# Kernel tuning notes

Measured on AMD Instinct MI355X. Metric: run time of the kernel, lower is better.

## Reference

```python
import jax, jax.numpy as jnp
import numpy as np

B, S, D = 4, 4096, 1024

def setup_inputs() -> dict:
    key = jax.random.key(0)
    ks = jax.random.split(key, 8)
    scale = 1.0 / np.sqrt(D)
    return {
        "inputs": jax.random.normal(ks[0], (B, S, D), dtype=jnp.float32),
        "context": jax.random.normal(ks[1], (B, S, D), dtype=jnp.float32),
        "Wq": jax.random.normal(ks[2], (D, D), dtype=jnp.float32) * scale,
        "bq": jnp.zeros((D,), dtype=jnp.float32),
        "Wk": jax.random.normal(ks[3], (D, D), dtype=jnp.float32) * scale,
        "bk": jnp.zeros((D,), dtype=jnp.float32),
        "Wv": jax.random.normal(ks[4], (D, D), dtype=jnp.float32) * scale,
        "bv": jnp.zeros((D,), dtype=jnp.float32),
        "Wo": jax.random.normal(ks[5], (D, D), dtype=jnp.float32) * scale,
        "bo": jnp.zeros((D,), dtype=jnp.float32),
    }

def reference(inputs, context, Wq, bq, Wk, bk, Wv, bv, Wo, bo):
    phi = lambda x: jax.nn.elu(x) + 1.0
    q_phi = phi(jnp.einsum("bsd,de->bse", inputs, Wq) + bq)   # [B,S,D]
    k_phi = phi(jnp.einsum("bsd,de->bse", context, Wk) + bk)  # [B,S,D]
    v = jnp.einsum("bsd,de->bse", context, Wv) + bv           # [B,S,D]
    kv = jnp.einsum("bsd,bse->bde", k_phi, v)                 # [B,D,D]
    k_sum = jnp.sum(k_phi, axis=1)                            # [B,D]
    z = 1.0 / (jnp.einsum("bsd,bd->bs", q_phi, k_sum)[..., None] + 1e-6)  # [B,S,1]
    out = jnp.einsum("bsd,bde->bse", q_phi, kv) * z           # [B,S,D]
    return jnp.einsum("bsd,de->bse", out, Wo) + bo + inputs
```

## Files before the change

### kernel.cpp

```cpp
#include <hip/hip_runtime.h>


typedef __bf16 bf16x8 __attribute__((ext_vector_type(8)));
typedef __bf16 bf16x4 __attribute__((ext_vector_type(4)));
typedef float  f32x4  __attribute__((ext_vector_type(4)));

#define GLOBAL_AS __attribute__((address_space(1)))
#define LDS_AS    __attribute__((address_space(3)))

#define SS 4096
#define DD 1024

__device__ __forceinline__ __bf16 f2bf(float f) {
  union { float f; unsigned u; } a; a.f = f;
  unsigned r = a.u + 0x7FFFu + ((a.u >> 16) & 1u);
  union { unsigned short s; __bf16 b; } o; o.s = (unsigned short)(r >> 16);
  return o.b;
}

__device__ __forceinline__ void async_load16(const void* g, void* l) {
  __builtin_amdgcn_global_load_lds((const GLOBAL_AS void*)g, (LDS_AS void*)l, 16, 0, 0);
}


#define LA0 0
#define LA1 16384
#define LB0 32768
#define LB1 49152

#define VMW(n)  asm volatile("s_waitcnt vmcnt(" #n ")" ::: "memory")
#define SBAR()  asm volatile("s_barrier" ::: "memory")
#define LGK0()  do { asm volatile("s_waitcnt lgkmcnt(0)" ::: "memory"); \
                     __builtin_amdgcn_sched_barrier(0); } while (0)

#define STG_A(BASE, mh, kt) do {                                              \
    async_load16(Aa + (long)((mh)*64 + t6) * K + (kt)*64 + gc8,               \
                 smem + (BASE) + (mh)*8192 + tid*8);                          \
    async_load16(Aa + (long)(128 + (mh)*64 + t6) * K + (kt)*64 + gc8,         \
                 smem + (BASE) + (mh)*8192 + 4096 + tid*8);                   \
  } while (0)

#define STG_B(BASE, nh, kt) do {                                              \
    async_load16(Bb + (long)(tA*64 + (nh)*32 + t5) * K + (kt)*64 + gc8,       \
                 smem + (BASE) + (nh)*8192 + tid*8);                          \
    async_load16(Bb + (long)(128 + tA*64 + (nh)*32 + t5) * K + (kt)*64 + gc8, \
                 smem + (BASE) + (nh)*8192 + 4096 + tid*8);                   \
  } while (0)

#define RD_A(dst, AB, mh)                                                     \
    _Pragma("unroll") for (int rr = 0; rr < 4; ++rr) {                        \
      const int o = (AB) + (mh)*8192 + rr*1024 + aoff;                        \
      dst[rr][0] = *(const bf16x8*)(smem + o);                                \
      dst[rr][1] = *(const bf16x8*)(smem + (o ^ 32));                         \
    }

#define RD_B(dst, BB, nh)                                                     \
    _Pragma("unroll") for (int nn = 0; nn < 2; ++nn) {                        \
      const int o = (BB) + (nh)*8192 + nn*1024 + boff;                        \
      dst[nn][0] = *(const bf16x8*)(smem + o);                                \
      dst[nn][1] = *(const bf16x8*)(smem + (o ^ 32));                         \
    }

#define MM(mh, nh, af, bf)                                                    \
    __builtin_amdgcn_s_setprio(1);                                            \
    _Pragma("unroll") for (int rr = 0; rr < 4; ++rr)                          \
    _Pragma("unroll") for (int nn = 0; nn < 2; ++nn) {                        \
      acc[(mh)*4+rr][(nh)*2+nn] = __builtin_amdgcn_mfma_f32_16x16x32_bf16(    \
          af[rr][0], bf[nn][0], acc[(mh)*4+rr][(nh)*2+nn], 0, 0, 0);          \
      acc[(mh)*4+rr][(nh)*2+nn] = __builtin_amdgcn_mfma_f32_16x16x32_bf16(    \
          af[rr][1], bf[nn][1], acc[(mh)*4+rr][(nh)*2+nn], 0, 0, 0);          \
    }                                                                         \
    __builtin_amdgcn_s_setprio(0)

#define PH(VM, RDS, STG, MMM) do {                                            \
    VM; RDS; STG;                                                             \
    SBAR();                                                                   \
    LGK0();                                                                   \
    MMM;                                                                      \
    SBAR();                                                                   \
  } while (0)

template<int MODE>
__global__ __launch_bounds__(512, 2)
void gemm256(const __bf16* __restrict__ Ag, const __bf16* __restrict__ Bg,
             void* __restrict__ Cg, void* __restrict__ Cg2,
             int N, int K, long sB,
             const float* __restrict__ bias, const float* __restrict__ bias2,
             const float* __restrict__ zvec, const float* __restrict__ resid)
{
  union SMem {
    __bf16 st[65536];
    __bf16 T[256 * 136];
  };
  __shared__ SMem sm;
  __bf16* smem = sm.st;

  int bx = blockIdx.x, by = blockIdx.y;
  {
    const int gx = gridDim.x, gy = gridDim.y;
    if ((gy & 7) == 0) {
      const int f = by * gx + bx;
      const int j = f & 7;
      const int u = f >> 3;
      bx = u % gx;
      by = j * (gy >> 3) + u / gx;
    }
  }

  const int tid  = threadIdx.x;
  const int lane = tid & 63, wave = tid >> 6;
  const int wm   = wave >> 2, wn = wave & 3;
  const int ln   = lane & 15, quad = lane >> 4;
  const int t6   = tid >> 3, tA = t6 >> 5, t5 = t6 & 31;
  const int gc8  = ((tid & 7) ^ (t6 & 7)) * 8;
  const int pco  = (quad ^ (ln & 7)) * 8;
  const int aoff = (wm * 64 + ln) * 64 + pco;
  const int boff = (wn * 32 + ln) * 64 + pco;

  const long m0  = (long)by * 256;
  const int  n0g = bx * 256;
  const __bf16* Aa = Ag + m0 * K;
  const __bf16* Bb = Bg + (long)bx * 256 * K +
                     ((MODE == 8) ? (long)(m0 >> 12) * sB : 0);

  f32x4 acc[8][4];
  const f32x4 zero = {0.f, 0.f, 0.f, 0.f};
#pragma unroll
  for (int i = 0; i < 8; i++)
#pragma unroll
    for (int j = 0; j < 4; j++) acc[i][j] = zero;

  STG_A(LA0, 0, 0); STG_B(LB0, 0, 0);
  STG_A(LA0, 1, 0); STG_B(LB0, 1, 0);
  STG_A(LA1, 0, 1); STG_B(LB1, 0, 1);
  VMW(8);
  SBAR();

  const int niter = K >> 7;
#pragma unroll 1
  for (int i = 0; i < niter - 1; ++i) {
    const int kb = i * 2;
    bf16x8 a[4][2], b[2][2], b1[2][2];
    PH(VMW(4), RD_A(a, LA0, 0) RD_B(b, LB0, 0), STG_A(LA1, 1, kb + 1), MM(0, 0, a, b));
    PH(      , RD_B(b1, LB0, 1),                STG_B(LB1, 1, kb + 1), MM(0, 1, a, b1));
    PH(      , RD_A(a, LA0, 1) RD_B(b, LB0, 0), STG_A(LA0, 0, kb + 2), MM(1, 0, a, b));
    PH(VMW(6), RD_B(b1, LB0, 1),                STG_B(LB0, 0, kb + 2), MM(1, 1, a, b1));
    PH(VMW(4), RD_A(a, LA1, 0) RD_B(b, LB1, 0), STG_A(LA0, 1, kb + 2), MM(0, 0, a, b));
    PH(      , RD_B(b1, LB1, 1),                STG_B(LB0, 1, kb + 2), MM(0, 1, a, b1));
    PH(      , RD_A(a, LA1, 1) RD_B(b, LB1, 0), STG_A(LA1, 0, kb + 3), MM(1, 0, a, b));
    PH(VMW(6), RD_B(b1, LB1, 1),                STG_B(LB1, 0, kb + 3), MM(1, 1, a, b1));
  }
  {
    const int kb = (niter - 1) * 2;
    bf16x8 a[4][2], b[2][2], b1[2][2];
    PH(VMW(4), RD_A(a, LA0, 0) RD_B(b, LB0, 0), STG_A(LA1, 1, kb + 1), MM(0, 0, a, b));
    PH(      , RD_B(b1, LB0, 1),                STG_B(LB1, 1, kb + 1), MM(0, 1, a, b1));
    PH(      , RD_A(a, LA0, 1) RD_B(b, LB0, 0), ,                      MM(1, 0, a, b));
    PH(VMW(0), RD_B(b1, LB0, 1),                ,                      MM(1, 1, a, b1));
    PH(      , RD_A(a, LA1, 0) RD_B(b, LB1, 0), ,                      MM(0, 0, a, b));
    PH(      , RD_B(b1, LB1, 1),                ,                      MM(0, 1, a, b1));
    PH(      , RD_A(a, LA1, 1) RD_B(b, LB1, 0), ,                      MM(1, 0, a, b));
    PH(      , RD_B(b1, LB1, 1),                ,                      MM(1, 1, a, b1));
  }

  if (MODE == 6) {
    const bool isK = (n0g < 1024);
    const float* bb = isK ? bias : bias2;
    const int nb = isK ? n0g : (n0g - 1024);
    const int b = (int)(m0 >> 12);
    const long s_in = m0 & 4095;
    __bf16* dst = (__bf16*)(isK ? Cg : Cg2) + (long)b * DD * SS;
#pragma unroll
    for (int h = 0; h < 2; ++h) {
      if (wm == h) {
#pragma unroll
        for (int mf = 0; mf < 8; ++mf)
#pragma unroll
          for (int nf = 0; nf < 4; ++nf) {
            const int nl = wn * 64 + nf * 16 + ln;
            const int sl0 = mf * 16 + quad * 4;
            const float bv = bb[nb + nl];
            bf16x4 pk;
#pragma unroll
            for (int r = 0; r < 4; ++r) {
              float x = acc[mf][nf][r] + bv;
              if (isK) x = (x > 0.f) ? (x + 1.f) : __expf(x);
              pk[r] = f2bf(x);
            }
            *(bf16x4*)(sm.T + nl * 136 + sl0) = pk;
          }
      }
      __syncthreads();
#pragma unroll
      for (int p2 = 0; p2 < 8; ++p2) {
        const int row = (tid >> 4) + p2 * 32;
        const int c   = (tid & 15) * 8;
        bf16x8 vv = *(const bf16x8*)(sm.T + row * 136 + c);
        *(bf16x8*)&dst[(long)(nb + row) * SS + s_in + h * 128 + c] = vv;
      }
      __syncthreads();
    }
    return;
  }

#pragma unroll
  for (int mf = 0; mf < 8; ++mf)
#pragma unroll
    for (int nf = 0; nf < 4; ++nf)
#pragma unroll
      for (int r = 0; r < 4; ++r) {
        const long gm = m0 + wm * 128 + mf * 16 + quad * 4 + r;
        const int  gn = n0g + wn * 64 + nf * 16 + ln;
        float x = acc[mf][nf][r];
        if (MODE == 0) {
          x += bias[gn];
          x = (x > 0.f) ? (x + 1.f) : __expf(x);
          ((__bf16*)Cg)[gm * (long)N + gn] = f2bf(x);
        } else {
          x = x * zvec[gm] + bias[gn];
          ((float*)Cg)[gm * (long)N + gn] = x + resid[gm * (long)N + gn];
        }
      }
}

#undef PH
#undef MM
#undef RD_A
#undef RD_B
#undef STG_A
#undef STG_B

template<int MODE>
__global__ __launch_bounds__(256)
void gemm_bt(const __bf16* __restrict__ Ag, const __bf16* __restrict__ Bg,
             void* __restrict__ Cg, void* __restrict__ Cg2,
             int N, int K, long sA, long sB, long sC,
             const float* __restrict__ bias, const float* __restrict__ bias2,
             const float* __restrict__ zvec,
             const float* __restrict__ resid)
{
  union SMem {
    struct { __bf16 As[128 * 64]; __bf16 Bs[128 * 64]; } s;
    __bf16 T[128 * 136];
  };
  __shared__ SMem sm;

  int bx = blockIdx.x, by = blockIdx.y;
  {
    const int gx = gridDim.x, gy = gridDim.y;
    if ((gy & 7) == 0) {
      const int f = by * gx + bx;
      const int j = f & 7;
      const int u = f >> 3;
      bx = u % gx;
      by = j * (gy >> 3) + u / gx;
    }
  }
  int bz = blockIdx.z;
  int k0beg = 0, k0end = K;
  if (MODE == 5) {
    const int split = bz & 3;
    bz >>= 2;
    k0beg = split * (K >> 2);
    k0end = k0beg + (K >> 2);
  }

  const int tid = threadIdx.x;
  const long m0 = (long)by * 128;
  const __bf16* A = Ag + m0 * K + bz * sA;
  const __bf16* B = Bg + (long)bx * 128 * K + bz * sB;

  const int srow = tid >> 3;
  const int gcc8 = ((tid & 7) ^ (srow & 7)) * 8;

  const int lane = tid & 63;
  const int wave = tid >> 6;
  const int wm   = (wave >> 1) * 64;
  const int wn   = (wave & 1) * 64;
  const int ln   = lane & 15;
  const int quad = lane >> 4;
  const int rk   = ln & 7;

  f32x4 acc[4][4];
  const f32x4 zero = {0.f, 0.f, 0.f, 0.f};
#pragma unroll
  for (int i = 0; i < 4; i++)
#pragma unroll
    for (int j = 0; j < 4; j++) acc[i][j] = zero;

  for (int k0 = k0beg; k0 < k0end; k0 += 64) {
#pragma unroll
    for (int p = 0; p < 4; p++) {
      async_load16(A + (long)(p * 32 + srow) * K + k0 + gcc8, sm.s.As + p * 2048 + tid * 8);
      async_load16(B + (long)(p * 32 + srow) * K + k0 + gcc8, sm.s.Bs + p * 2048 + tid * 8);
    }
    __syncthreads();

#pragma unroll
    for (int ksub = 0; ksub < 2; ksub++) {
      const int cc = (ksub * 4 + quad) ^ rk;
      bf16x8 af[4], bfr[4];
#pragma unroll
      for (int i = 0; i < 4; i++)
        af[i] = *(const bf16x8*)(sm.s.As + (wm + i * 16 + ln) * 64 + cc * 8);
#pragma unroll
      for (int j = 0; j < 4; j++)
        bfr[j] = *(const bf16x8*)(sm.s.Bs + (wn + j * 16 + ln) * 64 + cc * 8);
#pragma unroll
      for (int i = 0; i < 4; i++)
#pragma unroll
        for (int j = 0; j < 4; j++)
          acc[i][j] = __builtin_amdgcn_mfma_f32_16x16x32_bf16(af[i], bfr[j], acc[i][j], 0, 0, 0);
    }
    __syncthreads();
  }

  const int n0g = bx * 128;
#pragma unroll
  for (int i = 0; i < 4; i++) {
#pragma unroll
    for (int j = 0; j < 4; j++) {
#pragma unroll
      for (int r = 0; r < 4; r++) {
        const int lrow = wm + i * 16 + quad * 4 + r;
        const int lcol = wn + j * 16 + ln;
        const long gm  = m0 + lrow;
        const int  gn  = n0g + lcol;
        float x = acc[i][j][r];
        if (MODE == 5) {
          __hip_atomic_fetch_add(&((float*)Cg)[(long)bz * sC + gm * (long)N + gn],
                                 x, __ATOMIC_RELAXED, __HIP_MEMORY_SCOPE_AGENT);
        } else if (MODE == 7) {
          ((__bf16*)Cg)[(long)bz * sC + gm * (long)N + gn] = f2bf(x);
        }
      }
    }
  }
}

__global__ __launch_bounds__(256)
void cvt_f32_bf16(const float* __restrict__ x, __bf16* __restrict__ y, long n)
{
  long i = ((long)blockIdx.x * 256 + threadIdx.x) * 4;
  if (i < n) {
    float4 v = *(const float4*)(x + i);
    bf16x4 o;
    o[0] = f2bf(v.x); o[1] = f2bf(v.y); o[2] = f2bf(v.z); o[3] = f2bf(v.w);
    *(bf16x4*)(y + i) = o;
  }
}

__global__ __launch_bounds__(256)
void wtrans(const float* W0, const float* W1, const float* W2, const float* W3,
            __bf16* O0, __bf16* O1, __bf16* O2, __bf16* O3, int Dd)
{
  __shared__ __bf16 t[64][72];
  const float* W = (blockIdx.z == 0) ? W0 : (blockIdx.z == 1) ? W1 : (blockIdx.z == 2) ? W2 : W3;
  __bf16*      O = (blockIdx.z == 0) ? O0 : (blockIdx.z == 1) ? O1 : (blockIdx.z == 2) ? O2 : O3;
  const int r0 = blockIdx.y * 64, c0 = blockIdx.x * 64;
  const int tid = threadIdx.x;
  const int lr4 = tid >> 4, lc4 = (tid & 15) * 4;
#pragma unroll
  for (int it = 0; it < 4; it++) {
    const int row = lr4 + it * 16;
    float4 v = *(const float4*)&W[(long)(r0 + row) * Dd + c0 + lc4];
    t[row][lc4 + 0] = f2bf(v.x);
    t[row][lc4 + 1] = f2bf(v.y);
    t[row][lc4 + 2] = f2bf(v.z);
    t[row][lc4 + 3] = f2bf(v.w);
  }
  __syncthreads();
  const int lr8 = tid >> 3, lc8 = (tid & 7) * 8;
#pragma unroll
  for (int it = 0; it < 2; it++) {
    const int orow = lr8 + it * 32;
    bf16x8 vb;
#pragma unroll
    for (int j = 0; j < 8; j++) vb[j] = t[lc8 + j][orow];
    *(bf16x8*)&O[(long)(c0 + orow) * Dd + r0 + lc8] = vb;
  }
}

__global__ __launch_bounds__(256)
void ksum_k(const __bf16* __restrict__ kphiT, float* __restrict__ ksum, int S)
{
  const long row = blockIdx.x;
  const __bf16* p = kphiT + row * (long)S;
  const int tid = threadIdx.x;
  float s = 0.f;
  for (int j = tid * 8; j < S; j += 256 * 8) {
    bf16x8 v = *(const bf16x8*)&p[j];
#pragma unroll
    for (int e = 0; e < 8; e++) s += (float)v[e];
  }
  __shared__ float red[256];
  red[tid] = s; __syncthreads();
  for (int off = 128; off > 0; off >>= 1) {
    if (tid < off) red[tid] += red[tid + off];
    __syncthreads();
  }
  if (tid == 0) ksum[row] = red[0];
}

__global__ __launch_bounds__(256)
void zden_k(const __bf16* __restrict__ qphi, const float* __restrict__ ksum,
            float* __restrict__ z, int Dd, int S)
{
  const long row = blockIdx.x;
  const int  b   = (int)(row / S);
  const __bf16* q = qphi + row * (long)Dd;
  const float* ks = ksum + (long)b * Dd;
  const int tid = threadIdx.x;
  const int i = tid * 4;
  bf16x4 qv = *(const bf16x4*)&q[i];
  float4 kv4 = *(const float4*)&ks[i];
  float s = (float)qv[0] * kv4.x + (float)qv[1] * kv4.y +
            (float)qv[2] * kv4.z + (float)qv[3] * kv4.w;
  __shared__ float red[256];
  red[tid] = s; __syncthreads();
  for (int off = 128; off > 0; off >>= 1) {
    if (tid < off) red[tid] += red[tid + off];
    __syncthreads();
  }
  if (tid == 0) z[row] = 1.f / (red[0] + 1e-6f);
}

extern "C" void kernel_launch(void* const* d_in, const int* in_sizes, int n_in,
                              void* d_out, int out_size, void* d_ws, size_t ws_size,
                              hipStream_t stream)
{
  const float* inputs  = (const float*)d_in[0];
  const float* context = (const float*)d_in[1];
  const float* Wq = (const float*)d_in[2];
  const float* bq = (const float*)d_in[3];
  const float* Wk = (const float*)d_in[4];
  const float* bk = (const float*)d_in[5];
  const float* Wv = (const float*)d_in[6];
  const float* bv = (const float*)d_in[7];
  const float* Wo = (const float*)d_in[8];
  const float* bo = (const float*)d_in[9];
  float* out = (float*)d_out;

  const int Bn = 4;
  const long NSD = (long)Bn * SS * DD;
  const long MB = 1L << 20;

  char* ws = (char*)d_ws;
  __bf16* xbf   = (__bf16*)(ws + 0 * MB);
  __bf16* cbf   = (__bf16*)(ws + 32 * MB);
  __bf16* qphi  = (__bf16*)(ws + 64 * MB);
  __bf16* kphiT = (__bf16*)(ws + 96 * MB);
  __bf16* vT    = (__bf16*)(ws + 128 * MB);
  float*  kvf   = (float*)(ws + 160 * MB);
  __bf16* kvbf  = (__bf16*)(ws + 176 * MB);
  __bf16* M2T   = (__bf16*)(ws + 184 * MB);
  __bf16* WqT   = (__bf16*)(ws + 192 * MB);
  __bf16* WkT   = (__bf16*)(ws + 194 * MB);
  __bf16* WvT   = (__bf16*)(ws + 196 * MB);
  __bf16* WoT   = (__bf16*)(ws + 198 * MB);
  float*  ksum  = (float*)(ws + 200 * MB);
  float*  zbuf  = (float*)(ws + 201 * MB);

  cvt_f32_bf16<<<16384, 256, 0, stream>>>(inputs,  xbf, NSD);
  cvt_f32_bf16<<<16384, 256, 0, stream>>>(context, cbf, NSD);
  wtrans<<<dim3(16, 16, 4), 256, 0, stream>>>(Wq, Wk, Wv, Wo, WqT, WkT, WvT, WoT, DD);

  gemm256<0><<<dim3(4, 64), 512, 0, stream>>>(xbf, WqT, qphi, nullptr,
      DD, DD, 0, bq, nullptr, nullptr, nullptr);

  gemm256<6><<<dim3(8, 64), 512, 0, stream>>>(cbf, WkT, kphiT, vT,
      2048, DD, 0, bk, bv, nullptr, nullptr);

  ksum_k<<<4096, 256, 0, stream>>>(kphiT, ksum, SS);
  zden_k<<<16384, 256, 0, stream>>>(qphi, ksum, zbuf, DD, SS);

  hipMemsetAsync(kvf, 0, (size_t)Bn * DD * DD * sizeof(float), stream);
  gemm_bt<5><<<dim3(8, 8, 16), 256, 0, stream>>>(kphiT, vT, kvf, nullptr,
      DD, SS, (long)DD * SS, (long)DD * SS, (long)DD * DD,
      nullptr, nullptr, nullptr, nullptr);
  cvt_f32_bf16<<<4096, 256, 0, stream>>>(kvf, kvbf, (long)Bn * DD * DD);

  gemm_bt<7><<<dim3(8, 8, 4), 256, 0, stream>>>(WoT, kvbf, M2T, nullptr,
      DD, DD, 0, (long)DD * DD, (long)DD * DD, nullptr, nullptr, nullptr, nullptr);

  gemm256<8><<<dim3(4, 64), 512, 0, stream>>>(qphi, M2T, out, nullptr,
      DD, DD, (long)DD * DD, bo, nullptr, zbuf, inputs);
}
```

Measured before the change: 512.2 us.

## Halve GEMM main-loop barriers and reorder MFMA phases to reuse B fragments

The main loop and tail of the bf16 GEMM drop the trailing s_barrier and the explicit lgkmcnt(0)/sched_barrier from each phase, so each phase has one barrier. Async global-to-LDS staging is now issued before the LDS fragment reads. The MFMA sub-tile order in each half-iteration becomes (0,0),(0,1),(1,1),(1,0), so the B fragments already in registers are reused and two RD_B reloads per half-iteration are skipped. The goal is to cut barrier stalls and LDS read traffic. The risk is a write-after-read race on LDS buffers now that the second barrier is gone, plus less control over instruction scheduling.

```diff
diff --git a/kernel.cpp b/kernel.cpp
--- a/kernel.cpp
+++ b/kernel.cpp
@@ -30,8 +30,6 @@
 
 #define VMW(n)  asm volatile("s_waitcnt vmcnt(" #n ")" ::: "memory")
 #define SBAR()  asm volatile("s_barrier" ::: "memory")
-#define LGK0()  do { asm volatile("s_waitcnt lgkmcnt(0)" ::: "memory"); \
-                     __builtin_amdgcn_sched_barrier(0); } while (0)
 
 #define STG_A(BASE, mh, kt) do {                                              \
     async_load16(Aa + (long)((mh)*64 + t6) * K + (kt)*64 + gc8,               \
@@ -72,12 +70,10 @@
     }                                                                         \
     __builtin_amdgcn_s_setprio(0)
 
-#define PH(VM, RDS, STG, MMM) do {                                            \
-    VM; RDS; STG;                                                             \
+#define PH(VM, STG, RDS, MMM) do {                                            \
+    VM; STG; RDS;                                                             \
     SBAR();                                                                   \
-    LGK0();                                                                   \
     MMM;                                                                      \
-    SBAR();                                                                   \
   } while (0)
 
 template<int MODE>
@@ -141,26 +137,27 @@
   for (int i = 0; i < niter - 1; ++i) {
     const int kb = i * 2;
     bf16x8 a[4][2], b[2][2], b1[2][2];
-    PH(VMW(4), RD_A(a, LA0, 0) RD_B(b, LB0, 0), STG_A(LA1, 1, kb + 1), MM(0, 0, a, b));
-    PH(      , RD_B(b1, LB0, 1),                STG_B(LB1, 1, kb + 1), MM(0, 1, a, b1));
-    PH(      , RD_A(a, LA0, 1) RD_B(b, LB0, 0), STG_A(LA0, 0, kb + 2), MM(1, 0, a, b));
-    PH(VMW(6), RD_B(b1, LB0, 1),                STG_B(LB0, 0, kb + 2), MM(1, 1, a, b1));
-    PH(VMW(4), RD_A(a, LA1, 0) RD_B(b, LB1, 0), STG_A(LA0, 1, kb + 2), MM(0, 0, a, b));
-    PH(      , RD_B(b1, LB1, 1),                STG_B(LB0, 1, kb + 2), MM(0, 1, a, b1));
-    PH(      , RD_A(a, LA1, 1) RD_B(b, LB1, 0), STG_A(LA1, 0, kb + 3), MM(1, 0, a, b));
-    PH(VMW(6), RD_B(b1, LB1, 1),                STG_B(LB1, 0, kb + 3), MM(1, 1, a, b1));
+    PH(VMW(4), STG_A(LA1,1,kb+1), RD_A(a,LA0,0) RD_B(b,LB0,0), MM(0,0,a,b));
+    PH(      , STG_B(LB1,1,kb+1), RD_B(b1,LB0,1),              MM(0,1,a,b1));
+    PH(      , STG_A(LA0,0,kb+2), RD_A(a,LA0,1),               MM(1,1,a,b1));
+    PH(VMW(6), STG_B(LB0,0,kb+2), ,                            MM(1,0,a,b));
+    PH(VMW(4), STG_A(LA0,1,kb+2), RD_A(a,LA1,0) RD_B(b,LB1,0), MM(0,0,a,b));
+    PH(      , STG_B(LB0,1,kb+2), RD_B(b1,LB1,1),              MM(0,1,a,b1));
+    PH(      , STG_A(LA1,0,kb+3), RD_A(a,LA1,1),               MM(1,1,a,b1));
+    PH(VMW(6), STG_B(LB1,0,kb+3), ,                            MM(1,0,a,b));
   }
   {
     const int kb = (niter - 1) * 2;
     bf16x8 a[4][2], b[2][2], b1[2][2];
-    PH(VMW(4), RD_A(a, LA0, 0) RD_B(b, LB0, 0), STG_A(LA1, 1, kb + 1), MM(0, 0, a, b));
-    PH(      , RD_B(b1, LB0, 1),                STG_B(LB1, 1, kb + 1), MM(0, 1, a, b1));
-    PH(      , RD_A(a, LA0, 1) RD_B(b, LB0, 0), ,                      MM(1, 0, a, b));
-    PH(VMW(0), RD_B(b1, LB0, 1),                ,                      MM(1, 1, a, b1));
-    PH(      , RD_A(a, LA1, 0) RD_B(b, LB1, 0), ,                      MM(0, 0, a, b));
-    PH(      , RD_B(b1, LB1, 1),                ,                      MM(0, 1, a, b1));
-    PH(      , RD_A(a, LA1, 1) RD_B(b, LB1, 0), ,                      MM(1, 0, a, b));
-    PH(      , RD_B(b1, LB1, 1),                ,                      MM(1, 1, a, b1));
+    PH(VMW(4), STG_A(LA1,1,kb+1), RD_A(a,LA0,0) RD_B(b,LB0,0), MM(0,0,a,b));
+    PH(      , STG_B(LB1,1,kb+1), RD_B(b1,LB0,1),              MM(0,1,a,b1));
+    PH(      , ,                  RD_A(a,LA0,1),               MM(1,1,a,b1));
+    PH(VMW(0), ,                  ,                            MM(1,0,a,b));
+    PH(      , ,                  RD_A(a,LA1,0) RD_B(b,LB1,0), MM(0,0,a,b));
+    PH(      , ,                  RD_B(b1,LB1,1),              MM(0,1,a,b1));
+    PH(      , ,                  RD_A(a,LA1,1),               MM(1,1,a,b1));
+    PH(      , ,                  ,                            MM(1,0,a,b));
+    SBAR();
   }
 
   if (MODE == 6) {
```

Measured after the change: 515.3 us. No clear change (+0.6%).
